# Kernel optimization log

Measured on AMD Instinct MI355X. Metric: run time of the kernel, lower is better.

Reference implementation:

```python
import jax, jax.numpy as jnp
import numpy as np

B, N = 1, 768
C_S, C_Z, C_H, H, P_QK, P_V = 384, 128, 16, 12, 4, 8
INF = 100000.0
EPS = 1e-8


def _points(s, w, b, rot, trans, P):
    # PointProjection: linear -> [B,N,H,3,P] -> [B,N,H,P,3] local points,
    # then global = R @ p_local + t (rigid broadcast over heads/points).
    pl = (s @ w + b).reshape(s.shape[0], s.shape[1], H, 3, P)
    pl = jnp.moveaxis(pl, -2, -1)  # [B,N,H,P,3]
    return jnp.einsum('bnij,bnhpj->bnhpi', rot, pl) + trans[:, :, None, None, :]


def setup_inputs():
    key = jax.random.key(0)
    ks = jax.random.split(key, 14)

    def lin(k, fi, fo):
        k1, k2 = jax.random.split(k)
        w = jax.random.normal(k1, (fi, fo), jnp.float32) / np.float32(np.sqrt(fi))
        b = jax.random.normal(k2, (fo,), jnp.float32) * 0.01
        return w, b

    s = jax.random.normal(ks[0], (B, N, C_S), jnp.float32)
    z = jax.random.normal(ks[1], (B, N, N, C_Z), jnp.float32)
    rot = jnp.linalg.qr(jax.random.normal(ks[2], (B, N, 3, 3), jnp.float32))[0]
    trans = jax.random.normal(ks[3], (B, N, 3), jnp.float32)
    mask = jnp.ones((B, N), jnp.float32)

    w_q, b_q = lin(ks[4], C_S, H * C_H)
    w_k, b_k = lin(ks[5], C_S, H * C_H)
    w_v, b_v = lin(ks[6], C_S, H * C_H)
    w_qp, b_qp = lin(ks[7], C_S, H * 3 * P_QK)
    w_kp, b_kp = lin(ks[8], C_S, H * 3 * P_QK)
    w_vp, b_vp = lin(ks[9], C_S, H * 3 * P_V)
    w_b, b_b = lin(ks[10], C_Z, H)
    head_weights = jax.random.normal(ks[11], (H,), jnp.float32) * 0.1
    w_o, b_o = lin(ks[12], H * (C_Z + C_H + 4 * P_V), C_S)

    return dict(s=s, z=z, rot=rot, trans=trans, mask=mask,
                w_q=w_q, b_q=b_q, w_k=w_k, b_k=b_k, w_v=w_v, b_v=b_v,
                w_qp=w_qp, b_qp=b_qp, w_kp=w_kp, b_kp=b_kp, w_vp=w_vp, b_vp=b_vp,
                w_b=w_b, b_b=b_b, head_weights=head_weights, w_o=w_o, b_o=b_o)


def reference(s, z, rot, trans, mask,
              w_q, b_q, w_k, b_k, w_v, b_v,
              w_qp, b_qp, w_kp, b_kp, w_vp, b_vp,
              w_b, b_b, head_weights, w_o, b_o):
    # per-head point weights: sqrt(2 / (9 * P_QK)) * softplus(head_weights)
    pw = np.float32(np.sqrt(2.0 / (9.0 * P_QK))) * jnp.logaddexp(head_weights, 0.0)  # [H]

    q_pts = _points(s, w_qp, b_qp, rot, trans, P_QK)  # [B,N,H,P,3]
    k_pts = _points(s, w_kp, b_kp, rot, trans, P_QK)

    # sum_p ||q_p - k_p||^2 expanded: |q|^2 + |k|^2 - 2 q.k (summed over p,xyz)
    qk_pt = jnp.einsum('bqhpc,bkhpc->bqkh', q_pts, k_pts)
    q2 = jnp.sum(q_pts * q_pts, axis=(-2, -1))  # [B,N,H]
    k2 = jnp.sum(k_pts * k_pts, axis=(-2, -1))
    pt_att = -0.5 * pw * (q2[:, :, None, :] + k2[:, None, :, :] - 2.0 * qk_pt)  # [B,Nq,Nk,H]

    q = (s @ w_q + b_q).reshape(B, N, H, C_H) * np.float32(np.sqrt(1.0 / C_H))
    k = (s @ w_k + b_k).reshape(B, N, H, C_H)
    a = pt_att + jnp.einsum('bqhc,bkhc->bqkh', q, k)
    a = a + (z @ w_b + b_b)  # pair bias [B,Nq,Nk,H]

    sq_mask = mask[:, :, None] * mask[:, None, :]
    a = a + (INF * (sq_mask - 1.0))[..., None]
    a = jax.nn.softmax(a * np.float32(np.sqrt(1.0 / 3.0)), axis=-2)  # softmax over k

    v = (s @ w_v + b_v).reshape(B, N, H, C_H)
    o = jnp.einsum('bqkh,bkhc->bqhc', a, v).reshape(B, N, H * C_H)

    v_pts = _points(s, w_vp, b_vp, rot, trans, P_V)  # [B,N,H,P,3]
    o_pt = jnp.einsum('bqkh,bkhpc->bqhpc', a, v_pts).reshape(B, N, H * P_V, 3)
    # inverse rigid: R^T @ (p - t)
    o_pt = jnp.einsum('bnji,bnpj->bnpi', rot, o_pt - trans[:, :, None, :])  # [B,N,H*P_V,3]
    o_pt_norm = jnp.sqrt(jnp.sum(o_pt * o_pt, axis=-1) + EPS)  # [B,N,H*P_V]

    o_pair = jnp.einsum('bqkh,bqkc->bqhc', a, z).reshape(B, N, H * C_Z)

    cat = jnp.concatenate(
        [o, o_pt[..., 0], o_pt[..., 1], o_pt[..., 2], o_pt_norm, o_pair], axis=-1)
    return cat @ w_o + b_o  # [B,N,C_S]
```

## Files before the change

kernel.cpp:

```cpp
#include <hip/hip_runtime.h>
#include <math.h>

#define NN 768
#define KALL 1152
#define CATD 2112
#define INF_ 100000.0f

__device__ __forceinline__ float4 ld4(const float* p) { return *(const float4*)p; }

__global__ __launch_bounds__(256) void pack_kernel(
    const float* wq, const float* bq, const float* wk, const float* bk,
    const float* wv, const float* bv, const float* wqp, const float* bqp,
    const float* wkp, const float* bkp, const float* wvp, const float* bvp,
    float* Wall, float* ball) {
  int idx = blockIdx.x * 256 + threadIdx.x;
  if (idx >= 385 * KALL) return;
  int kk = idx / KALL, u = idx - kk * KALL;
  const float *w, *b; int col, dim; float sc = 1.f;
  if (u < 192)      { w = wq;  b = bq;  col = u;       dim = 192; sc = 0.25f; }
  else if (u < 384) { w = wk;  b = bk;  col = u - 192; dim = 192; }
  else if (u < 576) { w = wv;  b = bv;  col = u - 384; dim = 192; }
  else if (u < 720) { w = wqp; b = bqp; col = u - 576; dim = 144; }
  else if (u < 864) { w = wkp; b = bkp; col = u - 720; dim = 144; }
  else              { w = wvp; b = bvp; col = u - 864; dim = 288; }
  if (kk < 384) Wall[kk * KALL + u] = sc * w[kk * dim + col];
  else          ball[u] = sc * b[col];
}

__global__ __launch_bounds__(256) void proj_kernel(const float* s, const float* Wall,
                                                   const float* ball, float* proj) {
  int q0 = blockIdx.x * 32, c0 = blockIdx.y * 64;
  int tid = threadIdx.x;
  int qa = q0 + (tid >> 4) * 2, qb = qa + 1;
  int c = c0 + (tid & 15) * 4;
  const float* sa = s + qa * 384;
  const float* sb = s + qb * 384;
  const float* wp = Wall + c;
  float4 acc0 = {0, 0, 0, 0}, acc1 = {0, 0, 0, 0};
#pragma unroll 4
  for (int k = 0; k < 384; k++) {
    float4 w4 = ld4(wp + k * KALL);
    float a0 = sa[k], a1 = sb[k];
    acc0.x += a0 * w4.x; acc0.y += a0 * w4.y; acc0.z += a0 * w4.z; acc0.w += a0 * w4.w;
    acc1.x += a1 * w4.x; acc1.y += a1 * w4.y; acc1.z += a1 * w4.z; acc1.w += a1 * w4.w;
  }
  float4 b4 = ld4(ball + c);
  acc0.x += b4.x; acc0.y += b4.y; acc0.z += b4.z; acc0.w += b4.w;
  acc1.x += b4.x; acc1.y += b4.y; acc1.z += b4.z; acc1.w += b4.w;
  *(float4*)(proj + (size_t)qa * KALL + c) = acc0;
  *(float4*)(proj + (size_t)qb * KALL + c) = acc1;
}

__global__ __launch_bounds__(256) void points_kernel(const float* proj, const float* rot,
                                                     const float* trans, float* qpts, float* kpts,
                                                     float* vpts, float* q2, float* k2) {
  int n = blockIdx.x, tid = threadIdx.x;
  __shared__ float sq[12], sk[12];
  if (tid < 12) { sq[tid] = 0.f; sk[tid] = 0.f; }
  __syncthreads();
  if (tid < 192) {
    const float* R = rot + n * 9;
    const float* T = trans + n * 3;
    const float* pr = proj + (size_t)n * KALL;
    int base, P; float* outp; int h; bool isq = false, isk = false;
    if (tid < 48)      { h = tid >> 2; int p = tid & 3; base = 576 + h * 12; P = 4;
                         outp = qpts + n * 144 + h * 12 + p * 3; base += p; isq = true; }
    else if (tid < 96) { int i = tid - 48; h = i >> 2; int p = i & 3; base = 720 + h * 12; P = 4;
                         outp = kpts + n * 144 + h * 12 + p * 3; base += p; isk = true; }
    else               { int i = tid - 96; h = i >> 3; int p = i & 7; base = 864 + h * 24; P = 8;
                         outp = vpts + n * 288 + h * 24 + p * 3; base += p; }
    float l0 = pr[base], l1 = pr[base + P], l2 = pr[base + 2 * P];
    float g0 = R[0] * l0 + R[1] * l1 + R[2] * l2 + T[0];
    float g1 = R[3] * l0 + R[4] * l1 + R[5] * l2 + T[1];
    float g2 = R[6] * l0 + R[7] * l1 + R[8] * l2 + T[2];
    outp[0] = g0; outp[1] = g1; outp[2] = g2;
    float ns = g0 * g0 + g1 * g1 + g2 * g2;
    if (isq) atomicAdd(&sq[h], ns);
    else if (isk) atomicAdd(&sk[h], ns);
  }
  __syncthreads();
  if (tid < 12) { q2[n * 12 + tid] = sq[tid]; k2[n * 12 + tid] = sk[tid]; }
}

__global__ __launch_bounds__(256) void bias_kernel(const float* z, const float* wb,
                                                   const float* bb, float* abuf) {
  int q = blockIdx.x, k0 = blockIdx.y * 128;
  int tid = threadIdx.x;
  __shared__ float wsm[12 * 128];
  __shared__ float bbs[12];
  for (int i = tid; i < 1536; i += 256) { int hh = i >> 7, c = i & 127; wsm[i] = wb[c * 12 + hh]; }
  if (tid < 12) bbs[tid] = bb[tid];
  __syncthreads();
  int kl = tid & 127, h0 = tid >> 7;
  const float* zp = z + (size_t)(q * NN + k0 + kl) * 128;
  float acc[6] = {0, 0, 0, 0, 0, 0};
  for (int c4 = 0; c4 < 128; c4 += 4) {
    float4 z4 = ld4(zp + c4);
    const float zz[4] = {z4.x, z4.y, z4.z, z4.w};
#pragma unroll
    for (int cc = 0; cc < 4; cc++) {
      float zv = zz[cc];
#pragma unroll
      for (int j = 0; j < 6; j++) acc[j] += zv * wsm[(h0 + 2 * j) * 128 + c4 + cc];
    }
  }
#pragma unroll
  for (int j = 0; j < 6; j++) {
    int hh = h0 + 2 * j;
    abuf[((size_t)q * 12 + hh) * NN + k0 + kl] = acc[j] + bbs[hh];
  }
}

__global__ __launch_bounds__(256) void softmax_kernel(const float* proj, const float* qpts,
                                                      const float* kpts, const float* q2,
                                                      const float* k2, const float* mask,
                                                      const float* hw, float* abuf) {
  int q0 = blockIdx.x * 8, h = blockIdx.y;
  int tid = threadIdx.x;
  __shared__ float qw[8][16], qp[8][12], q2s[8], mq[8], red[4][8], row[8], pws;
  if (tid < 128) qw[tid >> 4][tid & 15] = proj[(size_t)(q0 + (tid >> 4)) * KALL + h * 16 + (tid & 15)];
  else if (tid < 224) { int i = tid - 128; qp[i / 12][i % 12] = qpts[(q0 + i / 12) * 144 + h * 12 + i % 12]; }
  else if (tid < 232) q2s[tid - 224] = q2[(q0 + tid - 224) * 12 + h];
  else if (tid < 240) mq[tid - 232] = mask[q0 + tid - 232];
  else if (tid == 240) {
    float x = hw[h];
    pws = 0.23570226039551584f * (fmaxf(x, 0.f) + log1pf(__expf(-fabsf(x))));
  }
  __syncthreads();

  float L[3][8];
#pragma unroll
  for (int i = 0; i < 3; i++) {
    int kk = i * 256 + tid;
    float kw[16], kp[12];
    const float* kwp = proj + (size_t)kk * KALL + 192 + h * 16;
    *(float4*)(kw) = ld4(kwp); *(float4*)(kw + 4) = ld4(kwp + 4);
    *(float4*)(kw + 8) = ld4(kwp + 8); *(float4*)(kw + 12) = ld4(kwp + 12);
    const float* kpp = kpts + (size_t)kk * 144 + h * 12;
    *(float4*)(kp) = ld4(kpp); *(float4*)(kp + 4) = ld4(kpp + 4); *(float4*)(kp + 8) = ld4(kpp + 8);
    float k2v = k2[kk * 12 + h];
    float mk = mask[kk];
#pragma unroll
    for (int q = 0; q < 8; q++) {
      float d = 0.f, dp = 0.f;
#pragma unroll
      for (int j = 0; j < 16; j++) d += qw[q][j] * kw[j];
#pragma unroll
      for (int j = 0; j < 12; j++) dp += qp[q][j] * kp[j];
      float bias = abuf[((size_t)(q0 + q) * 12 + h) * NN + kk];
      float val = bias + d - 0.5f * pws * (q2s[q] + k2v - 2.f * dp) + INF_ * (mq[q] * mk - 1.f);
      L[i][q] = val * 0.5773502691896258f;
    }
  }
  float m[8];
#pragma unroll
  for (int q = 0; q < 8; q++) m[q] = fmaxf(fmaxf(L[0][q], L[1][q]), L[2][q]);
#pragma unroll
  for (int d = 1; d < 64; d <<= 1)
#pragma unroll
    for (int q = 0; q < 8; q++) m[q] = fmaxf(m[q], __shfl_xor(m[q], d, 64));
  int wv = tid >> 6;
  if ((tid & 63) == 0)
    for (int q = 0; q < 8; q++) red[wv][q] = m[q];
  __syncthreads();
  if (tid < 8) row[tid] = fmaxf(fmaxf(red[0][tid], red[1][tid]), fmaxf(red[2][tid], red[3][tid]));
  __syncthreads();
  float sm[8];
#pragma unroll
  for (int q = 0; q < 8; q++) {
    float mm = row[q];
    L[0][q] = __expf(L[0][q] - mm);
    L[1][q] = __expf(L[1][q] - mm);
    L[2][q] = __expf(L[2][q] - mm);
    sm[q] = L[0][q] + L[1][q] + L[2][q];
  }
#pragma unroll
  for (int d = 1; d < 64; d <<= 1)
#pragma unroll
    for (int q = 0; q < 8; q++) sm[q] += __shfl_xor(sm[q], d, 64);
  if ((tid & 63) == 0)
    for (int q = 0; q < 8; q++) red[wv][q] = sm[q];
  __syncthreads();
  if (tid < 8) row[tid] = 1.f / (red[0][tid] + red[1][tid] + red[2][tid] + red[3][tid]);
  __syncthreads();
#pragma unroll
  for (int q = 0; q < 8; q++) {
    float r = row[q];
    float* ap = abuf + ((size_t)(q0 + q) * 12 + h) * NN + tid;
    ap[0] = L[0][q] * r; ap[256] = L[1][q] * r; ap[512] = L[2][q] * r;
  }
}

__global__ __launch_bounds__(256) void opair_kernel(const float* z, const float* abuf, float* cat) {
  int q = blockIdx.x, tid = threadIdx.x;
  int c = tid & 127, h0 = tid >> 7;
  const float* zp = z + (size_t)q * NN * 128 + c;
  const float* ap = abuf + (size_t)q * 12 * NN;
  float acc[6] = {0, 0, 0, 0, 0, 0};
  for (int k4 = 0; k4 < NN; k4 += 4) {
    float4 av[6];
#pragma unroll
    for (int j = 0; j < 6; j++) av[j] = ld4(ap + (h0 + 2 * j) * NN + k4);
#pragma unroll
    for (int kk = 0; kk < 4; kk++) {
      float zv = zp[(size_t)(k4 + kk) * 128];
      const float* avf;
#pragma unroll
      for (int j = 0; j < 6; j++) {
        avf = (const float*)&av[j];
        acc[j] += zv * avf[kk];
      }
    }
  }
#pragma unroll
  for (int j = 0; j < 6; j++)
    cat[(size_t)q * CATD + 576 + (h0 + 2 * j) * 128 + c] = acc[j];
}

__global__ __launch_bounds__(256) void ov_kernel(const float* proj, const float* vpts,
                                                 const float* abuf, const float* rot,
                                                 const float* trans, float* cat) {
  int h = blockIdx.x, q0 = blockIdx.y * 32;
  int tid = threadIdx.x;
  int qg = tid >> 3, jb = tid & 7;
  int q = q0 + qg;
  const float* ap = abuf + ((size_t)q * 12 + h) * NN;
  const float* vp = proj + 384 + h * 16;
  const float* vpp = vpts + h * 24;
  float acc[5] = {0, 0, 0, 0, 0};
  for (int k = 0; k < NN; k += 4) {
    float4 a4 = ld4(ap + k);
    const float af[4] = {a4.x, a4.y, a4.z, a4.w};
#pragma unroll
    for (int kk = 0; kk < 4; kk++) {
      float av = af[kk];
      size_t kr = k + kk;
      acc[0] += av * vp[kr * KALL + jb];
      acc[1] += av * vp[kr * KALL + jb + 8];
      acc[2] += av * vpp[kr * 288 + jb];
      acc[3] += av * vpp[kr * 288 + jb + 8];
      acc[4] += av * vpp[kr * 288 + jb + 16];
    }
  }
  float* cq = cat + (size_t)q * CATD;
  cq[h * 16 + jb] = acc[0];
  cq[h * 16 + jb + 8] = acc[1];
  __shared__ float g[32][24];
  g[qg][jb] = acc[2]; g[qg][jb + 8] = acc[3]; g[qg][jb + 16] = acc[4];
  __syncthreads();
  int ql = tid >> 3, p = tid & 7;
  int qq = q0 + ql;
  float gx = g[ql][p * 3], gy = g[ql][p * 3 + 1], gz = g[ql][p * 3 + 2];
  const float* R = rot + qq * 9;
  const float* T = trans + qq * 3;
  float dx = gx - T[0], dy = gy - T[1], dz = gz - T[2];
  float lx = R[0] * dx + R[3] * dy + R[6] * dz;
  float ly = R[1] * dx + R[4] * dy + R[7] * dz;
  float lz = R[2] * dx + R[5] * dy + R[8] * dz;
  float nrm = sqrtf(lx * lx + ly * ly + lz * lz + 1e-8f);
  int hp = h * 8 + p;
  float* co = cat + (size_t)qq * CATD;
  co[192 + hp] = lx; co[288 + hp] = ly; co[384 + hp] = lz; co[480 + hp] = nrm;
}

__global__ __launch_bounds__(256) void out_part_kernel(const float* cat, const float* wo,
                                                       float* part) {
  int q0 = blockIdx.x * 16, c0 = blockIdx.y * 64, k0 = blockIdx.z * 264;
  int tid = threadIdx.x;
  int q = q0 + (tid >> 4);
  int c = c0 + (tid & 15) * 4;
  const float* cp = cat + (size_t)q * CATD + k0;
  const float* wp = wo + (size_t)k0 * 384 + c;
  float4 acc = {0, 0, 0, 0};
#pragma unroll 8
  for (int k = 0; k < 264; k++) {
    float a = cp[k];
    float4 w4 = ld4(wp + (size_t)k * 384);
    acc.x += a * w4.x; acc.y += a * w4.y; acc.z += a * w4.z; acc.w += a * w4.w;
  }
  *(float4*)(part + ((size_t)blockIdx.z * 768 + q) * 384 + c) = acc;
}

__global__ __launch_bounds__(256) void out_reduce_kernel(const float* part, const float* bo,
                                                         float* out) {
  int idx = blockIdx.x * 256 + threadIdx.x;
  int q = idx / 96, cg = idx - q * 96;
  int c = cg * 4;
  float4 acc = ld4(bo + c);
#pragma unroll
  for (int j = 0; j < 8; j++) {
    float4 p = ld4(part + ((size_t)j * 768 + q) * 384 + c);
    acc.x += p.x; acc.y += p.y; acc.z += p.z; acc.w += p.w;
  }
  *(float4*)(out + (size_t)q * 384 + c) = acc;
}

extern "C" void kernel_launch(void* const* d_in, const int* in_sizes, int n_in,
                              void* d_out, int out_size, void* d_ws, size_t ws_size,
                              hipStream_t stream) {
  const float* s     = (const float*)d_in[0];
  const float* z     = (const float*)d_in[1];
  const float* rot   = (const float*)d_in[2];
  const float* trans = (const float*)d_in[3];
  const float* mask  = (const float*)d_in[4];
  const float* wq    = (const float*)d_in[5];
  const float* bq    = (const float*)d_in[6];
  const float* wk    = (const float*)d_in[7];
  const float* bk    = (const float*)d_in[8];
  const float* wv    = (const float*)d_in[9];
  const float* bv    = (const float*)d_in[10];
  const float* wqp   = (const float*)d_in[11];
  const float* bqp   = (const float*)d_in[12];
  const float* wkp   = (const float*)d_in[13];
  const float* bkp   = (const float*)d_in[14];
  const float* wvp   = (const float*)d_in[15];
  const float* bvp   = (const float*)d_in[16];
  const float* wb    = (const float*)d_in[17];
  const float* bb    = (const float*)d_in[18];
  const float* hw    = (const float*)d_in[19];
  const float* wo    = (const float*)d_in[20];
  const float* bo    = (const float*)d_in[21];
  float* out = (float*)d_out;

  float* ws = (float*)d_ws;
  float* proj  = ws;
  float* Wall  = proj + 884736;
  float* ball  = Wall + 442368;
  float* qpts  = ball + 1152;
  float* kpts  = qpts + 110592;
  float* vpts  = kpts + 110592;
  float* q2    = vpts + 221184;
  float* k2    = q2 + 9216;
  float* abuf  = k2 + 9216;
  float* cat   = abuf + 7077888;
  float* part  = cat + 1622016;

  pack_kernel<<<dim3((385 * KALL + 255) / 256), 256, 0, stream>>>(
      wq, bq, wk, bk, wv, bv, wqp, bqp, wkp, bkp, wvp, bvp, Wall, ball);
  proj_kernel<<<dim3(24, 18), 256, 0, stream>>>(s, Wall, ball, proj);
  points_kernel<<<dim3(768), 256, 0, stream>>>(proj, rot, trans, qpts, kpts, vpts, q2, k2);
  bias_kernel<<<dim3(768, 6), 256, 0, stream>>>(z, wb, bb, abuf);
  softmax_kernel<<<dim3(96, 12), 256, 0, stream>>>(proj, qpts, kpts, q2, k2, mask, hw, abuf);
  opair_kernel<<<dim3(768), 256, 0, stream>>>(z, abuf, cat);
  ov_kernel<<<dim3(12, 24), 256, 0, stream>>>(proj, vpts, abuf, rot, trans, cat);
  out_part_kernel<<<dim3(48, 6, 8), 256, 0, stream>>>(cat, wo, part);
  out_reduce_kernel<<<dim3(288), 256, 0, stream>>>(part, bo, out);
}
```

Measured before the change: 927.0 us.

## Rework pair-bias kernel, split ov reduction over k, vectorize softmax dot products

The pair-bias kernel now has each thread compute all 12 heads for three keys, reading a packed, zero-padded weight matrix through float4 loads instead of per-head shared-memory lookups. Its grid shrinks to one block per query. The ov kernel is split into a partial kernel over four k-chunks, so its 288 blocks become 1152, plus a reduce kernel that also applies the inverse rigid transform and norm. The softmax dot products read the query vectors as float4 from shared memory. The changes aim to cut weight-load traffic and raise parallelism in the small ov grid, at the cost of an extra launch and a partial buffer.

```diff
diff --git a/kernel.cpp b/kernel.cpp
--- a/kernel.cpp
+++ b/kernel.cpp
@@ -5,6 +5,7 @@
 #define KALL 1152
 #define CATD 2112
 #define INF_ 100000.0f
+#define PACKN (385 * KALL)
 
 __device__ __forceinline__ float4 ld4(const float* p) { return *(const float4*)p; }
 
@@ -12,9 +13,15 @@
     const float* wq, const float* bq, const float* wk, const float* bk,
     const float* wv, const float* bv, const float* wqp, const float* bqp,
     const float* wkp, const float* bkp, const float* wvp, const float* bvp,
-    float* Wall, float* ball) {
+    const float* wbm, float* Wall, float* ball, float* wpack) {
   int idx = blockIdx.x * 256 + threadIdx.x;
-  if (idx >= 385 * KALL) return;
+  if (idx >= PACKN + 2048) return;
+  if (idx >= PACKN) {
+    int u = idx - PACKN;
+    int c = u >> 4, hh = u & 15;
+    wpack[u] = (hh < 12) ? wbm[c * 12 + hh] : 0.f;
+    return;
+  }
   int kk = idx / KALL, u = idx - kk * KALL;
   const float *w, *b; int col, dim; float sc = 1.f;
   if (u < 192)      { w = wq;  b = bq;  col = u;       dim = 192; sc = 0.25f; }
@@ -82,32 +89,48 @@
   if (tid < 12) { q2[n * 12 + tid] = sq[tid]; k2[n * 12 + tid] = sk[tid]; }
 }
 
-__global__ __launch_bounds__(256) void bias_kernel(const float* z, const float* wb,
-                                                   const float* bb, float* abuf) {
-  int q = blockIdx.x, k0 = blockIdx.y * 128;
-  int tid = threadIdx.x;
-  __shared__ float wsm[12 * 128];
-  __shared__ float bbs[12];
-  for (int i = tid; i < 1536; i += 256) { int hh = i >> 7, c = i & 127; wsm[i] = wb[c * 12 + hh]; }
-  if (tid < 12) bbs[tid] = bb[tid];
-  __syncthreads();
-  int kl = tid & 127, h0 = tid >> 7;
-  const float* zp = z + (size_t)(q * NN + k0 + kl) * 128;
-  float acc[6] = {0, 0, 0, 0, 0, 0};
-  for (int c4 = 0; c4 < 128; c4 += 4) {
-    float4 z4 = ld4(zp + c4);
-    const float zz[4] = {z4.x, z4.y, z4.z, z4.w};
+__global__ __launch_bounds__(256) void bias_kernel(const float* __restrict__ z,
+                                                   const float* __restrict__ wpack,
+                                                   const float* __restrict__ bb,
+                                                   float* __restrict__ abuf) {
+  int q = blockIdx.x;
+  int kl = threadIdx.x;
+  const float* zp0 = z + ((size_t)q * NN + kl) * 128;
+  float acc0[12], acc1[12], acc2[12];
+#pragma unroll
+  for (int h = 0; h < 12; h++) { acc0[h] = 0.f; acc1[h] = 0.f; acc2[h] = 0.f; }
+  for (int c = 0; c < 128; c += 4) {
+    float4 z0 = ld4(zp0 + c);
+    float4 z1 = ld4(zp0 + 256 * 128 + c);
+    float4 z2 = ld4(zp0 + 512 * 128 + c);
+    const float zc0[4] = {z0.x, z0.y, z0.z, z0.w};
+    const float zc1[4] = {z1.x, z1.y, z1.z, z1.w};
+    const float zc2[4] = {z2.x, z2.y, z2.z, z2.w};
+    const float* wp = wpack + c * 16;
 #pragma unroll
     for (int cc = 0; cc < 4; cc++) {
-      float zv = zz[cc];
-#pragma unroll
-      for (int j = 0; j < 6; j++) acc[j] += zv * wsm[(h0 + 2 * j) * 128 + c4 + cc];
-    }
-  }
-#pragma unroll
-  for (int j = 0; j < 6; j++) {
-    int hh = h0 + 2 * j;
-    abuf[((size_t)q * 12 + hh) * NN + k0 + kl] = acc[j] + bbs[hh];
+      float4 wA = ld4(wp + cc * 16);
+      float4 wB = ld4(wp + cc * 16 + 4);
+      float4 wC = ld4(wp + cc * 16 + 8);
+      float v0 = zc0[cc], v1 = zc1[cc], v2 = zc2[cc];
+      acc0[0] += v0 * wA.x; acc0[1] += v0 * wA.y; acc0[2] += v0 * wA.z; acc0[3] += v0 * wA.w;
+      acc0[4] += v0 * wB.x; acc0[5] += v0 * wB.y; acc0[6] += v0 * wB.z; acc0[7] += v0 * wB.w;
+      acc0[8] += v0 * wC.x; acc0[9] += v0 * wC.y; acc0[10] += v0 * wC.z; acc0[11] += v0 * wC.w;
+      acc1[0] += v1 * wA.x; acc1[1] += v1 * wA.y; acc1[2] += v1 * wA.z; acc1[3] += v1 * wA.w;
+      acc1[4] += v1 * wB.x; acc1[5] += v1 * wB.y; acc1[6] += v1 * wB.z; acc1[7] += v1 * wB.w;
+      acc1[8] += v1 * wC.x; acc1[9] += v1 * wC.y; acc1[10] += v1 * wC.z; acc1[11] += v1 * wC.w;
+      acc2[0] += v2 * wA.x; acc2[1] += v2 * wA.y; acc2[2] += v2 * wA.z; acc2[3] += v2 * wA.w;
+      acc2[4] += v2 * wB.x; acc2[5] += v2 * wB.y; acc2[6] += v2 * wB.z; acc2[7] += v2 * wB.w;
+      acc2[8] += v2 * wC.x; acc2[9] += v2 * wC.y; acc2[10] += v2 * wC.z; acc2[11] += v2 * wC.w;
+    }
+  }
+#pragma unroll
+  for (int h = 0; h < 12; h++) {
+    float b = bb[h];
+    float* ap = abuf + ((size_t)q * 12 + h) * NN + kl;
+    ap[0] = acc0[h] + b;
+    ap[256] = acc1[h] + b;
+    ap[512] = acc2[h] + b;
   }
 }
 
@@ -142,11 +165,20 @@
     float mk = mask[kk];
 #pragma unroll
     for (int q = 0; q < 8; q++) {
-      float d = 0.f, dp = 0.f;
-#pragma unroll
-      for (int j = 0; j < 16; j++) d += qw[q][j] * kw[j];
-#pragma unroll
-      for (int j = 0; j < 12; j++) dp += qp[q][j] * kp[j];
+      float4 qa = *(const float4*)&qw[q][0];
+      float4 qb = *(const float4*)&qw[q][4];
+      float4 qc = *(const float4*)&qw[q][8];
+      float4 qd = *(const float4*)&qw[q][12];
+      float4 pa = *(const float4*)&qp[q][0];
+      float4 pb = *(const float4*)&qp[q][4];
+      float4 pc = *(const float4*)&qp[q][8];
+      float d = qa.x * kw[0] + qa.y * kw[1] + qa.z * kw[2] + qa.w * kw[3]
+              + qb.x * kw[4] + qb.y * kw[5] + qb.z * kw[6] + qb.w * kw[7]
+              + qc.x * kw[8] + qc.y * kw[9] + qc.z * kw[10] + qc.w * kw[11]
+              + qd.x * kw[12] + qd.y * kw[13] + qd.z * kw[14] + qd.w * kw[15];
+      float dp = pa.x * kp[0] + pa.y * kp[1] + pa.z * kp[2] + pa.w * kp[3]
+               + pb.x * kp[4] + pb.y * kp[5] + pb.z * kp[6] + pb.w * kp[7]
+               + pc.x * kp[8] + pc.y * kp[9] + pc.z * kp[10] + pc.w * kp[11];
       float bias = abuf[((size_t)(q0 + q) * 12 + h) * NN + kk];
       float val = bias + d - 0.5f * pws * (q2s[q] + k2v - 2.f * dp) + INF_ * (mq[q] * mk - 1.f);
       L[i][q] = val * 0.5773502691896258f;
@@ -217,18 +249,17 @@
     cat[(size_t)q * CATD + 576 + (h0 + 2 * j) * 128 + c] = acc[j];
 }
 
-__global__ __launch_bounds__(256) void ov_kernel(const float* proj, const float* vpts,
-                                                 const float* abuf, const float* rot,
-                                                 const float* trans, float* cat) {
-  int h = blockIdx.x, q0 = blockIdx.y * 32;
+__global__ __launch_bounds__(256) void ovpart_kernel(const float* proj, const float* vpts,
+                                                     const float* abuf, float* pov) {
+  int h = blockIdx.x, q0 = blockIdx.y * 32, kz = blockIdx.z;
   int tid = threadIdx.x;
   int qg = tid >> 3, jb = tid & 7;
   int q = q0 + qg;
-  const float* ap = abuf + ((size_t)q * 12 + h) * NN;
-  const float* vp = proj + 384 + h * 16;
-  const float* vpp = vpts + h * 24;
+  const float* ap = abuf + ((size_t)q * 12 + h) * NN + kz * 192;
+  const float* vp = proj + (size_t)(kz * 192) * KALL + 384 + h * 16;
+  const float* vpp = vpts + (size_t)(kz * 192) * 288 + h * 24;
   float acc[5] = {0, 0, 0, 0, 0};
-  for (int k = 0; k < NN; k += 4) {
+  for (int k = 0; k < 192; k += 4) {
     float4 a4 = ld4(ap + k);
     const float af[4] = {a4.x, a4.y, a4.z, a4.w};
 #pragma unroll
@@ -242,25 +273,49 @@
       acc[4] += av * vpp[kr * 288 + jb + 16];
     }
   }
-  float* cq = cat + (size_t)q * CATD;
-  cq[h * 16 + jb] = acc[0];
-  cq[h * 16 + jb + 8] = acc[1];
-  __shared__ float g[32][24];
-  g[qg][jb] = acc[2]; g[qg][jb + 8] = acc[3]; g[qg][jb + 16] = acc[4];
-  __syncthreads();
-  int ql = tid >> 3, p = tid & 7;
-  int qq = q0 + ql;
-  float gx = g[ql][p * 3], gy = g[ql][p * 3 + 1], gz = g[ql][p * 3 + 2];
-  const float* R = rot + qq * 9;
-  const float* T = trans + qq * 3;
-  float dx = gx - T[0], dy = gy - T[1], dz = gz - T[2];
-  float lx = R[0] * dx + R[3] * dy + R[6] * dz;
-  float ly = R[1] * dx + R[4] * dy + R[7] * dz;
-  float lz = R[2] * dx + R[5] * dy + R[8] * dz;
-  float nrm = sqrtf(lx * lx + ly * ly + lz * lz + 1e-8f);
-  int hp = h * 8 + p;
-  float* co = cat + (size_t)qq * CATD;
-  co[192 + hp] = lx; co[288 + hp] = ly; co[384 + hp] = lz; co[480 + hp] = nrm;
+  float* o = pov + (((size_t)kz * 768 + q) * 12 + h) * 40;
+  o[jb] = acc[0]; o[jb + 8] = acc[1];
+  o[16 + jb] = acc[2]; o[16 + jb + 8] = acc[3]; o[16 + jb + 16] = acc[4];
+}
+
+__global__ __launch_bounds__(256) void ovred_kernel(const float* pov, const float* rot,
+                                                    const float* trans, float* cat) {
+  int q = blockIdx.x, tid = threadIdx.x;
+  const float* pq = pov + (size_t)q * 480;
+  if (tid < 96) {
+    int h = tid >> 3, p = tid & 7;
+    float x = 0.f, y = 0.f, zz = 0.f;
+#pragma unroll
+    for (int j = 0; j < 4; j++) {
+      const float* b = pq + (size_t)j * 768 * 480 + h * 40 + 16 + p * 3;
+      x += b[0]; y += b[1]; zz += b[2];
+    }
+    const float* R = rot + q * 9;
+    const float* T = trans + q * 3;
+    float dx = x - T[0], dy = y - T[1], dz = zz - T[2];
+    float lx = R[0] * dx + R[3] * dy + R[6] * dz;
+    float ly = R[1] * dx + R[4] * dy + R[7] * dz;
+    float lz = R[2] * dx + R[5] * dy + R[8] * dz;
+    float nrm = sqrtf(lx * lx + ly * ly + lz * lz + 1e-8f);
+    int hp = h * 8 + p;
+    float* co = cat + (size_t)q * CATD;
+    co[192 + hp] = lx; co[288 + hp] = ly; co[384 + hp] = lz; co[480 + hp] = nrm;
+  } else {
+    int i = tid - 96;
+    int h = i >> 4, c = i & 15;
+    float s = 0.f;
+#pragma unroll
+    for (int j = 0; j < 4; j++) s += pq[(size_t)j * 768 * 480 + h * 40 + c];
+    cat[(size_t)q * CATD + h * 16 + c] = s;
+    if (i < 32) {
+      int i2 = i + 160;
+      int h2 = i2 >> 4, c2 = i2 & 15;
+      float s2 = 0.f;
+#pragma unroll
+      for (int j = 0; j < 4; j++) s2 += pq[(size_t)j * 768 * 480 + h2 * 40 + c2];
+      cat[(size_t)q * CATD + h2 * 16 + c2] = s2;
+    }
+  }
 }
 
 __global__ __launch_bounds__(256) void out_part_kernel(const float* cat, const float* wo,
@@ -334,15 +389,18 @@
   float* abuf  = k2 + 9216;
   float* cat   = abuf + 7077888;
   float* part  = cat + 1622016;
-
-  pack_kernel<<<dim3((385 * KALL + 255) / 256), 256, 0, stream>>>(
-      wq, bq, wk, bk, wv, bv, wqp, bqp, wkp, bkp, wvp, bvp, Wall, ball);
+  float* wpack = part + 2359296;
+  float* pov   = wpack + 2048;
+
+  pack_kernel<<<dim3((PACKN + 2048 + 255) / 256), 256, 0, stream>>>(
+      wq, bq, wk, bk, wv, bv, wqp, bqp, wkp, bkp, wvp, bvp, wb, Wall, ball, wpack);
   proj_kernel<<<dim3(24, 18), 256, 0, stream>>>(s, Wall, ball, proj);
   points_kernel<<<dim3(768), 256, 0, stream>>>(proj, rot, trans, qpts, kpts, vpts, q2, k2);
-  bias_kernel<<<dim3(768, 6), 256, 0, stream>>>(z, wb, bb, abuf);
+  bias_kernel<<<dim3(768), 256, 0, stream>>>(z, wpack, bb, abuf);
   softmax_kernel<<<dim3(96, 12), 256, 0, stream>>>(proj, qpts, kpts, q2, k2, mask, hw, abuf);
   opair_kernel<<<dim3(768), 256, 0, stream>>>(z, abuf, cat);
-  ov_kernel<<<dim3(12, 24), 256, 0, stream>>>(proj, vpts, abuf, rot, trans, cat);
+  ovpart_kernel<<<dim3(12, 24, 4), 256, 0, stream>>>(proj, vpts, abuf, pov);
+  ovred_kernel<<<dim3(768), 256, 0, stream>>>(pov, rot, trans, cat);
   out_part_kernel<<<dim3(48, 6, 8), 256, 0, stream>>>(cat, wo, part);
   out_reduce_kernel<<<dim3(288), 256, 0, stream>>>(part, bo, out);
 }
```

Result: slower. 1.068 ms (+15.2%).
